# Optimization experiments

Measured on AMD Instinct MI355X. Metric: run time of the kernel, lower is better.

The kernel has to match this reference:

```python
import jax, jax.numpy as jnp
import numpy as np

# ---- fixed sizes ----
N_IN = 100_000          # total inner nodes
NODES_PER_INNER = 50    # nodes per inner graph
N_OUT = N_IN // NODES_PER_INNER          # 2000 outer nodes (= num inner graphs)
NODES_PER_OUTER = 125   # outer nodes per outer graph
B = N_OUT // NODES_PER_OUTER             # 16 graphs in the batch
DEG = 8
E_IN = N_IN * DEG        # 800_000 inner edges
E_OUT = N_OUT * DEG      # 16_000 outer edges
IN_FEATS = 64
OUT_FEATS = 64
H = 128                  # h_feats = [128]*6
NUM_CLASSES = 10


def _rand_edges(key, n_graphs, nodes_per_graph, edges_per_graph):
    """Random edges that stay inside each graph of a batched graph."""
    k1, k2 = jax.random.split(key)
    src_l = jax.random.randint(k1, (n_graphs, edges_per_graph), 0, nodes_per_graph)
    dst_l = jax.random.randint(k2, (n_graphs, edges_per_graph), 0, nodes_per_graph)
    off = (jnp.arange(n_graphs) * nodes_per_graph)[:, None]
    return ((src_l + off).reshape(-1).astype(jnp.int32),
            (dst_l + off).reshape(-1).astype(jnp.int32))


def setup_inputs() -> dict:
    key = jax.random.key(0)
    ks = jax.random.split(key, 24)
    inner_src, inner_dst = _rand_edges(ks[0], N_OUT, NODES_PER_INNER, E_IN // N_OUT)
    outer_src, outer_dst = _rand_edges(ks[1], B, NODES_PER_OUTER, E_OUT // B)

    def w(k, fan_in, fan_out):
        return jax.random.normal(k, (fan_in, fan_out), jnp.float32) * (1.0 / np.sqrt(fan_in))

    inp = {
        "in_layer_feat": jax.random.normal(ks[2], (N_IN, IN_FEATS), jnp.float32),
        "out_layer_feat": jax.random.normal(ks[3], (N_OUT, OUT_FEATS), jnp.float32),
        "inner_ew": jax.random.uniform(ks[4], (E_IN,), jnp.float32) + 0.5,
        "outer_ew": jax.random.uniform(ks[5], (E_OUT,), jnp.float32) + 0.5,
        "W1": w(ks[6], IN_FEATS, H),        "b1": jnp.zeros((H,), jnp.float32),
        "W2": w(ks[7], H, H),               "b2": jnp.zeros((H,), jnp.float32),
        "W3": w(ks[8], OUT_FEATS + H, H),   "b3": jnp.zeros((H,), jnp.float32),
        "W4": w(ks[9], H, H),               "b4": jnp.zeros((H,), jnp.float32),
        "W5": w(ks[10], H, H),              "b5": jnp.zeros((H,), jnp.float32),
        "W6": w(ks[11], H, H),              "b6": jnp.zeros((H,), jnp.float32),
        "Wc": w(ks[12], H, NUM_CLASSES),    "bc": jnp.zeros((NUM_CLASSES,), jnp.float32),
        "inner_src": inner_src, "inner_dst": inner_dst,
        "outer_src": outer_src, "outer_dst": outer_dst,
        "inner_node_graph": (jnp.arange(N_IN) // NODES_PER_INNER).astype(jnp.int32),
        "outer_node_graph": (jnp.arange(N_OUT) // NODES_PER_OUTER).astype(jnp.int32),
    }
    return inp


def graph_conv(src, dst, ew, x, W, b, n_nodes):
    """DGL GraphConv, norm='both', weighted aggregation, zero-in-degree allowed."""
    ones = jnp.ones(src.shape[0], x.dtype)
    deg_out = jnp.clip(jax.ops.segment_sum(ones, src, num_segments=n_nodes), 1.0)
    deg_in = jnp.clip(jax.ops.segment_sum(ones, dst, num_segments=n_nodes), 1.0)
    xs = x * jax.lax.rsqrt(deg_out)[:, None]                      # src normalization
    msg = xs[src] * ew[:, None]                                   # u_mul_e
    agg = jax.ops.segment_sum(msg, dst, num_segments=n_nodes)     # copy_e -> sum
    agg = agg * jax.lax.rsqrt(deg_in)[:, None]                    # dst normalization
    return agg @ W + b


def mean_nodes(h, node_graph, n_graphs, nodes_per_graph):
    return jax.ops.segment_sum(h, node_graph, num_segments=n_graphs) / nodes_per_graph


def reference(in_layer_feat, out_layer_feat, inner_ew, outer_ew,
              W1, b1, W2, b2, W3, b3, W4, b4, W5, b5, W6, b6, Wc, bc,
              inner_src, inner_dst, outer_src, outer_dst,
              inner_node_graph, outer_node_graph):
    # inner-graph message passing
    h = jax.nn.relu(graph_conv(inner_src, inner_dst, inner_ew, in_layer_feat, W1, b1, N_IN))
    h = jax.nn.relu(graph_conv(inner_src, inner_dst, inner_ew, h, W2, b2, N_IN))
    reduced = mean_nodes(h, inner_node_graph, N_OUT, float(NODES_PER_INNER))  # [N_OUT, H]
    merged = jnp.concatenate([out_layer_feat, reduced], axis=-1)              # [N_OUT, OUT_FEATS+H]
    # outer-graph message passing
    h = jax.nn.relu(graph_conv(outer_src, outer_dst, outer_ew, merged, W3, b3, N_OUT))
    h = jax.nn.relu(graph_conv(outer_src, outer_dst, outer_ew, h, W4, b4, N_OUT))
    h = jax.nn.relu(graph_conv(outer_src, outer_dst, outer_ew, h, W5, b5, N_OUT))
    h = jax.nn.relu(graph_conv(outer_src, outer_dst, outer_ew, h, W6, b6, N_OUT))
    hg = mean_nodes(h, outer_node_graph, B, float(NODES_PER_OUTER))           # [B, H]
    return hg @ Wc + bc                                                       # [B, NUM_CLASSES]
```

## Files before the change

kernel.cpp:

```cpp
#include <hip/hip_runtime.h>

#define NPI 50
#define EPI 400
#define NPO 125
#define EPO 1000
#define N_IN 100000
#define N_OUT 2000
#define NB 16
#define NC 10

typedef _Float16 half_t;
typedef _Float16 f16x8 __attribute__((ext_vector_type(8)));
typedef float f32x4 __attribute__((ext_vector_type(4)));

#define MFMA(a, b, c) __builtin_amdgcn_mfma_f32_16x16x32_f16(a, b, c, 0, 0, 0)

__device__ __forceinline__ f16x8 lds_ld8(const half_t* base, int row, int k, int strideB) {
    return *(const f16x8*)((const char*)base + row * strideB + ((k * 2) ^ ((row & 7) << 4)));
}
__device__ __forceinline__ void lds_st1(half_t* base, int row, int col, int strideB, float v) {
    *(half_t*)((char*)base + row * strideB + ((col * 2) ^ ((row & 7) << 4))) = (half_t)v;
}
__device__ __forceinline__ void lds_st1h(half_t* base, int row, int col, int strideB, half_t v) {
    *(half_t*)((char*)base + row * strideB + ((col * 2) ^ ((row & 7) << 4))) = v;
}
__device__ __forceinline__ f16x8 scr_ld8(const half_t* base, int row, int k) {
    return *(const f16x8*)((const char*)base + row * 64 + ((k * 2) ^ ((row & 3) << 4)));
}
__device__ __forceinline__ void scr_st1(half_t* base, int row, int col, float v) {
    *(half_t*)((char*)base + row * 64 + ((col * 2) ^ ((row & 3) << 4))) = (half_t)v;
}

__global__ __launch_bounds__(256) void k_pre(
    const float* __restrict__ W1, const float* __restrict__ W2,
    const float* __restrict__ W3, const float* __restrict__ W4,
    const float* __restrict__ W5, const float* __restrict__ W6,
    half_t* __restrict__ WT1, half_t* __restrict__ WT2,
    half_t* __restrict__ WT3, half_t* __restrict__ WT4,
    half_t* __restrict__ WT5, half_t* __restrict__ WT6,
    const float* __restrict__ ew, const int* __restrict__ esrc,
    const int* __restrict__ edst, half_t* __restrict__ Aout)
{
    __shared__ float Af[NPO * NPO];
    __shared__ int cO[NPO], cI[NPO];
    __shared__ float rso[NPO], rsi[NPO];
    const int t = threadIdx.x;

    if (blockIdx.x < 384) {
        int i = blockIdx.x * 256 + t;
        const float* src; half_t* dst; int K;
        if      (i < 8192)  { src = W1; dst = WT1; K = 64; }
        else if (i < 24576) { src = W2; dst = WT2; K = 128; i -= 8192; }
        else if (i < 49152) { src = W3; dst = WT3; K = 192; i -= 24576; }
        else if (i < 65536) { src = W4; dst = WT4; K = 128; i -= 49152; }
        else if (i < 81920) { src = W5; dst = WT5; K = 128; i -= 65536; }
        else                { src = W6; dst = WT6; K = 128; i -= 81920; }
        int c = i & 127, k = i >> 7;
        dst[c * K + k] = (half_t)src[k * 128 + c];
        return;
    }

    const int g = blockIdx.x - 384;
    const int nb = g * NPO, eb = g * EPO;
    for (int i = t; i < NPO * NPO; i += 256) Af[i] = 0.f;
    if (t < NPO) { cO[t] = 0; cI[t] = 0; }
    __syncthreads();
    for (int e = t; e < EPO; e += 256) {
        int s = esrc[eb + e] - nb, d = edst[eb + e] - nb;
        atomicAdd(&Af[d * NPO + s], ew[eb + e]);
        atomicAdd(&cO[s], 1); atomicAdd(&cI[d], 1);
    }
    __syncthreads();
    if (t < NPO) {
        rso[t] = rsqrtf((float)max(cO[t], 1));
        rsi[t] = rsqrtf((float)max(cI[t], 1));
    }
    __syncthreads();
    for (int i = t; i < 128 * 16; i += 256) {
        int d = i >> 4, s0 = (i & 15) * 8;
        f16x8 v;
        #pragma unroll
        for (int j = 0; j < 8; j++) {
            int s = s0 + j;
            float x = (d < NPO && s < NPO) ? Af[d * NPO + s] * rsi[d] * rso[s] : 0.f;
            v[j] = (half_t)x;
        }
        *(f16x8*)&Aout[(size_t)g * 16384 + d * 128 + s0] = v;
    }
}

__global__ __launch_bounds__(256, 5) void k_inner(
    const float* __restrict__ X, const float* __restrict__ outfeat,
    const float* __restrict__ ew, const int* __restrict__ esrc,
    const int* __restrict__ edst,
    const half_t* __restrict__ WT1, const float* __restrict__ b1,
    const half_t* __restrict__ WT2, const float* __restrict__ b2,
    half_t* __restrict__ merged)
{
    __shared__ alignas(16) char smem[21504];
    half_t* R2  = (half_t*)smem;
    float*  Af  = (float*)smem;
    half_t* scr = (half_t*)(smem + 16384);
    float*  pool= (float*)(smem + 20480);
    int*    cO  = (int*)(smem + 20992);
    int*    cI  = (int*)(smem + 21248);

    const int g = blockIdx.x, t = threadIdx.x;
    const int w = t >> 6, l = t & 63, lr = l & 15, lk = l >> 4;
    const int nb = g * NPI, eb = g * EPI;
    half_t* scrw = scr + w * 512;

    float ofv = (t < 64) ? outfeat[(size_t)g * 64 + t] : 0.f;
    int s0e, d0e; float w0e;
    { int e = eb + t; s0e = esrc[e] - nb; d0e = edst[e] - nb; w0e = ew[e]; }
    int s1e = 0, d1e = 0; float w1e = 0.f;
    const bool e1v = (t + 256 < EPI);
    if (e1v) { int e = eb + t + 256; s1e = esrc[e] - nb; d1e = edst[e] - nb; w1e = ew[e]; }
    const int srow = t >> 2, qc = t & 3;
    f16x8 xh0 = {}, xh1 = {};
    if (srow < NPI) {
        const float* xp = &X[(size_t)(nb + srow) * 64 + qc * 16];
        float4 a = *(const float4*)(xp + 0), b = *(const float4*)(xp + 4);
        float4 c = *(const float4*)(xp + 8), d = *(const float4*)(xp + 12);
        xh0[0]=(half_t)a.x; xh0[1]=(half_t)a.y; xh0[2]=(half_t)a.z; xh0[3]=(half_t)a.w;
        xh0[4]=(half_t)b.x; xh0[5]=(half_t)b.y; xh0[6]=(half_t)b.z; xh0[7]=(half_t)b.w;
        xh1[0]=(half_t)c.x; xh1[1]=(half_t)c.y; xh1[2]=(half_t)c.z; xh1[3]=(half_t)c.w;
        xh1[4]=(half_t)d.x; xh1[5]=(half_t)d.y; xh1[6]=(half_t)d.z; xh1[7]=(half_t)d.w;
    }

    if (t < 64) { cO[t] = 0; cI[t] = 0; }
    if (t >= 64 && t < 192) pool[t - 64] = 0.f;
    for (int i = t; i < 4096; i += 256) Af[i] = 0.f;
    __syncthreads();

    atomicAdd(&Af[d0e * 64 + (s0e ^ ((d0e & 7) << 2))], w0e);
    atomicAdd(&cO[s0e], 1); atomicAdd(&cI[d0e], 1);
    if (e1v) {
        atomicAdd(&Af[d1e * 64 + (s1e ^ ((d1e & 7) << 2))], w1e);
        atomicAdd(&cO[s1e], 1); atomicAdd(&cI[d1e], 1);
    }
    __syncthreads();

    f16x8 afr[2];
    {
        const int r = w * 16 + lr;
        const int sw = (r & 7) << 2;
        const float rsi_l = rsqrtf((float)max(cI[r], 1));
        #pragma unroll
        for (int ks = 0; ks < 2; ks++) {
            const int c0 = ks * 32 + lk * 8;
            f32x4 v0 = *(const f32x4*)&Af[r * 64 + (c0 ^ sw)];
            f32x4 v1 = *(const f32x4*)&Af[r * 64 + ((c0 + 4) ^ sw)];
            f16x8 fr;
            #pragma unroll
            for (int j = 0; j < 4; j++)
                fr[j] = (half_t)(v0[j] * rsi_l * rsqrtf((float)max(cO[c0 + j], 1)));
            #pragma unroll
            for (int j = 0; j < 4; j++)
                fr[4 + j] = (half_t)(v1[j] * rsi_l * rsqrtf((float)max(cO[c0 + 4 + j], 1)));
            afr[ks] = fr;
        }
    }
    __syncthreads();

    #pragma unroll
    for (int i = 0; i < 8; i++) lds_st1h(R2, qc * 16 + i, srow, 128, xh0[i]);
    #pragma unroll
    for (int i = 0; i < 8; i++) lds_st1h(R2, qc * 16 + 8 + i, srow, 128, xh1[i]);
    __syncthreads();

    f32x4 hacc[8] = {};
    #pragma unroll
    for (int kf = 0; kf < 2; kf++) {
        f16x8 wb[8];
        #pragma unroll
        for (int nt = 0; nt < 8; nt++)
            wb[nt] = *(const f16x8*)&WT1[(nt * 16 + lr) * 64 + kf * 32 + lk * 8];
        #pragma unroll
        for (int j = 0; j < 2; j++) {
            const int ft = kf * 2 + j;
            f32x4 tacc = {};
            #pragma unroll
            for (int ks = 0; ks < 2; ks++) {
                f16x8 b = lds_ld8(R2, ft * 16 + lr, ks * 32 + lk * 8, 128);
                tacc = MFMA(afr[ks], b, tacc);
            }
            #pragma unroll
            for (int q = 0; q < 4; q++) scr_st1(scrw, lk * 4 + q, j * 16 + lr, tacc[q]);
        }
        f16x8 a1 = scr_ld8(scrw, lr, lk * 8);
        #pragma unroll
        for (int nt = 0; nt < 8; nt++) hacc[nt] = MFMA(a1, wb[nt], hacc[nt]);
    }
    __syncthreads();
    #pragma unroll
    for (int nt = 0; nt < 8; nt++) {
        int c = nt * 16 + lr;
        float bb = b1[c];
        #pragma unroll
        for (int q = 0; q < 4; q++)
            lds_st1(R2, c, w * 16 + lk * 4 + q, 128, fmaxf(hacc[nt][q] + bb, 0.f));
    }
    __syncthreads();

    f32x4 h2[8] = {};
    #pragma unroll
    for (int kf = 0; kf < 4; kf++) {
        f16x8 wb[8];
        #pragma unroll
        for (int nt = 0; nt < 8; nt++)
            wb[nt] = *(const f16x8*)&WT2[(nt * 16 + lr) * 128 + kf * 32 + lk * 8];
        #pragma unroll
        for (int j = 0; j < 2; j++) {
            const int ft = kf * 2 + j;
            f32x4 tacc = {};
            #pragma unroll
            for (int ks = 0; ks < 2; ks++) {
                f16x8 b = lds_ld8(R2, ft * 16 + lr, ks * 32 + lk * 8, 128);
                tacc = MFMA(afr[ks], b, tacc);
            }
            #pragma unroll
            for (int q = 0; q < 4; q++) scr_st1(scrw, lk * 4 + q, j * 16 + lr, tacc[q]);
        }
        f16x8 a1 = scr_ld8(scrw, lr, lk * 8);
        #pragma unroll
        for (int nt = 0; nt < 8; nt++) h2[nt] = MFMA(a1, wb[nt], h2[nt]);
    }
    #pragma unroll
    for (int nt = 0; nt < 8; nt++) {
        int c = nt * 16 + lr;
        float bb = b2[c];
        float ps = 0.f;
        #pragma unroll
        for (int q = 0; q < 4; q++) {
            int m = w * 16 + lk * 4 + q;
            float v = fmaxf(h2[nt][q] + bb, 0.f);
            ps += (m < NPI) ? v : 0.f;
        }
        ps += __shfl_xor(ps, 16);
        ps += __shfl_xor(ps, 32);
        if (lk == 0) atomicAdd(&pool[c], ps);
    }
    __syncthreads();
    if (t < 64) merged[(size_t)g * 192 + t] = (half_t)ofv;
    else if (t < 192) merged[(size_t)g * 192 + t] = (half_t)(pool[t - 64] * (1.f / NPI));
}

template <int FIN, bool STAGE, bool LAST>
__device__ __forceinline__ void outer_layer(
    const f16x8* afr, const half_t* __restrict__ mg,
    const half_t* __restrict__ WT, const float* __restrict__ bias,
    half_t* bufP, half_t* bufQ, float* pool,
    int wr, int wc, int lr, int lk, int t)
{
    f32x4 hacc[4] = {};
    constexpr int NCH = FIN / 64;
    f16x8 hv[NCH];
    if constexpr (STAGE) {
        const int s = t >> 3, fo = (t & 7) * 8;
        #pragma unroll
        for (int ch = 0; ch < NCH; ch++) {
            f16x8 z = {};
            hv[ch] = (s < NPO) ? *(const f16x8*)&mg[(size_t)s * 192 + ch * 64 + fo] : z;
        }
    }
    #pragma unroll
    for (int ch = 0; ch < NCH; ch++) {
        f16x8 wtb[8];
        #pragma unroll
        for (int ks2 = 0; ks2 < 2; ks2++)
            #pragma unroll
            for (int nt = 0; nt < 4; nt++)
                wtb[ks2 * 4 + nt] = *(const f16x8*)&WT[
                    (size_t)(wc * 64 + nt * 16 + lr) * FIN + ch * 64 + ks2 * 32 + lk * 8];
        if constexpr (STAGE) {
            const int s = t >> 3, fo = (t & 7) * 8;
            #pragma unroll
            for (int j = 0; j < 8; j++) lds_st1h(bufP, fo + j, s, 256, hv[ch][j]);
            __syncthreads();
        }
        const int rb = STAGE ? 0 : ch * 64;
        f32x4 tacc[2] = {};
        #pragma unroll
        for (int ks = 0; ks < 4; ks++) {
            #pragma unroll
            for (int nt = 0; nt < 2; nt++) {
                f16x8 b = lds_ld8(bufP, rb + wc * 32 + nt * 16 + lr, ks * 32 + lk * 8, 256);
                tacc[nt] = MFMA(afr[ks], b, tacc[nt]);
            }
        }
        #pragma unroll
        for (int nt = 0; nt < 2; nt++)
            #pragma unroll
            for (int q = 0; q < 4; q++)
                lds_st1(bufQ, wr * 16 + lk * 4 + q, wc * 32 + nt * 16 + lr, 128,
                        tacc[nt][q]);
        __syncthreads();
        #pragma unroll
        for (int ks2 = 0; ks2 < 2; ks2++) {
            f16x8 a1 = lds_ld8(bufQ, wr * 16 + lr, ks2 * 32 + lk * 8, 128);
            #pragma unroll
            for (int nt = 0; nt < 4; nt++)
                hacc[nt] = MFMA(a1, wtb[ks2 * 4 + nt], hacc[nt]);
        }
        __syncthreads();
    }
    if constexpr (!LAST) {
        #pragma unroll
        for (int nt = 0; nt < 4; nt++) {
            int c = wc * 64 + nt * 16 + lr;
            float bb = bias[c];
            #pragma unroll
            for (int q = 0; q < 4; q++)
                lds_st1(bufP, c, wr * 16 + lk * 4 + q, 256, fmaxf(hacc[nt][q] + bb, 0.f));
        }
        __syncthreads();
    } else {
        #pragma unroll
        for (int nt = 0; nt < 4; nt++) {
            int c = wc * 64 + nt * 16 + lr;
            float bb = bias[c];
            float ps = 0.f;
            #pragma unroll
            for (int q = 0; q < 4; q++) {
                int d = wr * 16 + lk * 4 + q;
                float v = fmaxf(hacc[nt][q] + bb, 0.f);
                ps += (d < NPO) ? v : 0.f;
            }
            ps += __shfl_xor(ps, 16);
            ps += __shfl_xor(ps, 32);
            if (lk == 0) atomicAdd(&pool[c], ps);
        }
        __syncthreads();
    }
}

__global__ __launch_bounds__(1024) void k_outer(
    const half_t* __restrict__ Aout, const half_t* __restrict__ merged,
    const half_t* __restrict__ WT3, const float* __restrict__ b3,
    const half_t* __restrict__ WT4, const float* __restrict__ b4,
    const half_t* __restrict__ WT5, const float* __restrict__ b5,
    const half_t* __restrict__ WT6, const float* __restrict__ b6,
    const float* __restrict__ Wc, const float* __restrict__ bc,
    float* __restrict__ out)
{
    __shared__ alignas(16) char smem[49704];
    half_t* bufP = (half_t*)smem;
    half_t* bufQ = (half_t*)(smem + 32768);
    float*  pool = (float*)(smem + 49152);
    float*  cls  = (float*)(smem + 49664);

    const int g = blockIdx.x, t = threadIdx.x;
    const int w = t >> 6, l = t & 63, lr = l & 15, lk = l >> 4;
    const int wr = w & 7, wc = w >> 3;
    const half_t* mg = merged + (size_t)g * NPO * 192;

    f16x8 afr[4];
    #pragma unroll
    for (int ks = 0; ks < 4; ks++)
        afr[ks] = *(const f16x8*)&Aout[(size_t)g * 16384
                                       + (wr * 16 + lr) * 128 + ks * 32 + lk * 8];
    if (t < 128) pool[t] = 0.f;
    if (t >= 128 && t < 128 + NC) cls[t - 128] = 0.f;
    __syncthreads();

    outer_layer<192, true,  false>(afr, mg, WT3, b3, bufP, bufQ, pool, wr, wc, lr, lk, t);
    outer_layer<128, false, false>(afr, nullptr, WT4, b4, bufP, bufQ, pool, wr, wc, lr, lk, t);
    outer_layer<128, false, false>(afr, nullptr, WT5, b5, bufP, bufQ, pool, wr, wc, lr, lk, t);
    outer_layer<128, false, true >(afr, nullptr, WT6, b6, bufP, bufQ, pool, wr, wc, lr, lk, t);

    if (t < 128) {
        float val = pool[t] * (1.f / NPO);
        float p[NC];
        #pragma unroll
        for (int c = 0; c < NC; c++) p[c] = val * Wc[t * NC + c];
        #pragma unroll
        for (int off = 32; off >= 1; off >>= 1)
            #pragma unroll
            for (int c = 0; c < NC; c++) p[c] += __shfl_xor(p[c], off);
        if ((t & 63) == 0)
            #pragma unroll
            for (int c = 0; c < NC; c++) atomicAdd(&cls[c], p[c]);
    }
    __syncthreads();
    if (t < NC) out[g * NC + t] = cls[t] + bc[t];
}

extern "C" void kernel_launch(void* const* d_in, const int* in_sizes, int n_in,
                              void* d_out, int out_size, void* d_ws, size_t ws_size,
                              hipStream_t stream)
{
    const float* X       = (const float*)d_in[0];
    const float* outfeat = (const float*)d_in[1];
    const float* iew     = (const float*)d_in[2];
    const float* oew     = (const float*)d_in[3];
    const float* W1 = (const float*)d_in[4];  const float* b1 = (const float*)d_in[5];
    const float* W2 = (const float*)d_in[6];  const float* b2 = (const float*)d_in[7];
    const float* W3 = (const float*)d_in[8];  const float* b3 = (const float*)d_in[9];
    const float* W4 = (const float*)d_in[10]; const float* b4 = (const float*)d_in[11];
    const float* W5 = (const float*)d_in[12]; const float* b5 = (const float*)d_in[13];
    const float* W6 = (const float*)d_in[14]; const float* b6 = (const float*)d_in[15];
    const float* Wc = (const float*)d_in[16]; const float* bc = (const float*)d_in[17];
    const int* isrc = (const int*)d_in[18];   const int* idst = (const int*)d_in[19];
    const int* osrc = (const int*)d_in[20];   const int* odst = (const int*)d_in[21];

    char* base = (char*)d_ws;
    half_t* WT1 = (half_t*)(base + 0);
    half_t* WT2 = (half_t*)(base + 16384);
    half_t* WT3 = (half_t*)(base + 49152);
    half_t* WT4 = (half_t*)(base + 98304);
    half_t* WT5 = (half_t*)(base + 131072);
    half_t* WT6 = (half_t*)(base + 163840);
    half_t* AoutG  = (half_t*)(base + 196608);
    half_t* merged = (half_t*)(base + 720896);

    k_pre<<<400, 256, 0, stream>>>(W1, W2, W3, W4, W5, W6,
                                   WT1, WT2, WT3, WT4, WT5, WT6,
                                   oew, osrc, odst, AoutG);
    k_inner<<<N_OUT, 256, 0, stream>>>(X, outfeat, iew, isrc, idst,
                                       WT1, b1, WT2, b2, merged);
    k_outer<<<NB, 1024, 0, stream>>>(AoutG, merged, WT3, b3, WT4, b4,
                                     WT5, b5, WT6, b6, Wc, bc, (float*)d_out);
}
```

Baseline: 122.3 us.

## Assign one inner graph per wavefront and drop block-level barriers

The inner-graph kernel now processes each inner graph with a single 64-lane wavefront, packing two graphs per 128-thread block, instead of a 256-thread block per graph. Each wave owns private LDS regions, so all __syncthreads and the pooled LDS atomics go away, and the mean pooling is done in registers with shuffles. Each wave loops over four 16-row tiles and keeps the adjacency fragments for all tiles in registers, with output-degree normalisation factors precomputed. This removes cross-wave barrier stalls, but it raises register pressure and LDS per block, lowers the number of waves per graph, and leans on wave-lockstep execution for LDS ordering.

```diff
diff --git a/kernel.cpp b/kernel.cpp
--- a/kernel.cpp
+++ b/kernel.cpp
@@ -89,7 +89,7 @@
     }
 }
 
-__global__ __launch_bounds__(256, 5) void k_inner(
+__global__ __launch_bounds__(128, 2) void k_inner(
     const float* __restrict__ X, const float* __restrict__ outfeat,
     const float* __restrict__ ew, const int* __restrict__ esrc,
     const int* __restrict__ edst,
@@ -97,53 +97,55 @@
     const half_t* __restrict__ WT2, const float* __restrict__ b2,
     half_t* __restrict__ merged)
 {
-    __shared__ alignas(16) char smem[21504];
-    half_t* R2  = (half_t*)smem;
-    float*  Af  = (float*)smem;
-    half_t* scr = (half_t*)(smem + 16384);
-    float*  pool= (float*)(smem + 20480);
-    int*    cO  = (int*)(smem + 20992);
-    int*    cI  = (int*)(smem + 21248);
-
-    const int g = blockIdx.x, t = threadIdx.x;
-    const int w = t >> 6, l = t & 63, lr = l & 15, lk = l >> 4;
+    __shared__ alignas(16) char smem[52224];
+    const int t = threadIdx.x, w = t >> 6, l = t & 63;
+    const int lr = l & 15, lk = l >> 4;
+    const int g = blockIdx.x * 2 + w;
+    char* R = smem + w * 26112;
+    float*  Af   = (float*)R;
+    half_t* h1T  = (half_t*)R;
+    half_t* XT   = (half_t*)(R + 16384);
+    half_t* scrw = (half_t*)(R + 24576);
+    int*    cO   = (int*)(R + 25600);
+    int*    cI   = (int*)(R + 25856);
     const int nb = g * NPI, eb = g * EPI;
-    half_t* scrw = scr + w * 512;
-
-    float ofv = (t < 64) ? outfeat[(size_t)g * 64 + t] : 0.f;
-    int s0e, d0e; float w0e;
-    { int e = eb + t; s0e = esrc[e] - nb; d0e = edst[e] - nb; w0e = ew[e]; }
-    int s1e = 0, d1e = 0; float w1e = 0.f;
-    const bool e1v = (t + 256 < EPI);
-    if (e1v) { int e = eb + t + 256; s1e = esrc[e] - nb; d1e = edst[e] - nb; w1e = ew[e]; }
-    const int srow = t >> 2, qc = t & 3;
-    f16x8 xh0 = {}, xh1 = {};
-    if (srow < NPI) {
-        const float* xp = &X[(size_t)(nb + srow) * 64 + qc * 16];
-        float4 a = *(const float4*)(xp + 0), b = *(const float4*)(xp + 4);
-        float4 c = *(const float4*)(xp + 8), d = *(const float4*)(xp + 12);
-        xh0[0]=(half_t)a.x; xh0[1]=(half_t)a.y; xh0[2]=(half_t)a.z; xh0[3]=(half_t)a.w;
-        xh0[4]=(half_t)b.x; xh0[5]=(half_t)b.y; xh0[6]=(half_t)b.z; xh0[7]=(half_t)b.w;
-        xh1[0]=(half_t)c.x; xh1[1]=(half_t)c.y; xh1[2]=(half_t)c.z; xh1[3]=(half_t)c.w;
-        xh1[4]=(half_t)d.x; xh1[5]=(half_t)d.y; xh1[6]=(half_t)d.z; xh1[7]=(half_t)d.w;
-    }
-
-    if (t < 64) { cO[t] = 0; cI[t] = 0; }
-    if (t >= 64 && t < 192) pool[t - 64] = 0.f;
-    for (int i = t; i < 4096; i += 256) Af[i] = 0.f;
-    __syncthreads();
-
-    atomicAdd(&Af[d0e * 64 + (s0e ^ ((d0e & 7) << 2))], w0e);
-    atomicAdd(&cO[s0e], 1); atomicAdd(&cI[d0e], 1);
-    if (e1v) {
-        atomicAdd(&Af[d1e * 64 + (s1e ^ ((d1e & 7) << 2))], w1e);
-        atomicAdd(&cO[s1e], 1); atomicAdd(&cI[d1e], 1);
-    }
-    __syncthreads();
-
-    f16x8 afr[2];
-    {
-        const int r = w * 16 + lr;
+
+    float ofv = outfeat[(size_t)g * 64 + l];
+    int se[7], de[7]; float wgt[7];
+    #pragma unroll
+    for (int i = 0; i < 7; i++) {
+        int e = l + i * 64;
+        if (e < EPI) {
+            se[i] = esrc[eb + e] - nb; de[i] = edst[eb + e] - nb; wgt[i] = ew[eb + e];
+        } else { se[i] = 0; de[i] = 0; wgt[i] = 0.f; }
+    }
+    float bb1[8], bb2[8];
+    #pragma unroll
+    for (int nt = 0; nt < 8; nt++) { bb1[nt] = b1[nt * 16 + lr]; bb2[nt] = b2[nt * 16 + lr]; }
+
+    cO[l] = 0; cI[l] = 0;
+    #pragma unroll
+    for (int i = 0; i < 16; i++)
+        *(f32x4*)&Af[(i * 64 + l) * 4] = (f32x4){0.f, 0.f, 0.f, 0.f};
+    #pragma unroll
+    for (int i = 0; i < 7; i++) {
+        if (l + i * 64 < EPI) {
+            atomicAdd(&Af[de[i] * 64 + (se[i] ^ ((de[i] & 7) << 2))], wgt[i]);
+            atomicAdd(&cO[se[i]], 1); atomicAdd(&cI[de[i]], 1);
+        }
+    }
+
+    float rso8[2][8];
+    #pragma unroll
+    for (int ks = 0; ks < 2; ks++)
+        #pragma unroll
+        for (int j = 0; j < 8; j++)
+            rso8[ks][j] = rsqrtf((float)max(cO[ks * 32 + lk * 8 + j], 1));
+
+    f16x8 afr[4][2];
+    #pragma unroll
+    for (int st = 0; st < 4; st++) {
+        const int r = st * 16 + lr;
         const int sw = (r & 7) << 2;
         const float rsi_l = rsqrtf((float)max(cI[r], 1));
         #pragma unroll
@@ -153,97 +155,109 @@
             f32x4 v1 = *(const f32x4*)&Af[r * 64 + ((c0 + 4) ^ sw)];
             f16x8 fr;
             #pragma unroll
-            for (int j = 0; j < 4; j++)
-                fr[j] = (half_t)(v0[j] * rsi_l * rsqrtf((float)max(cO[c0 + j], 1)));
-            #pragma unroll
-            for (int j = 0; j < 4; j++)
-                fr[4 + j] = (half_t)(v1[j] * rsi_l * rsqrtf((float)max(cO[c0 + 4 + j], 1)));
-            afr[ks] = fr;
-        }
-    }
-    __syncthreads();
-
-    #pragma unroll
-    for (int i = 0; i < 8; i++) lds_st1h(R2, qc * 16 + i, srow, 128, xh0[i]);
-    #pragma unroll
-    for (int i = 0; i < 8; i++) lds_st1h(R2, qc * 16 + 8 + i, srow, 128, xh1[i]);
-    __syncthreads();
-
-    f32x4 hacc[8] = {};
-    #pragma unroll
-    for (int kf = 0; kf < 2; kf++) {
-        f16x8 wb[8];
+            for (int j = 0; j < 4; j++) fr[j] = (half_t)(v0[j] * rsi_l * rso8[ks][j]);
+            #pragma unroll
+            for (int j = 0; j < 4; j++) fr[4 + j] = (half_t)(v1[j] * rsi_l * rso8[ks][4 + j]);
+            afr[st][ks] = fr;
+        }
+    }
+
+    #pragma unroll
+    for (int i = 0; i < 8; i++)
+        *(f32x4*)((char*)XT + (i * 64 + l) * 16) = (f32x4){0.f, 0.f, 0.f, 0.f};
+    for (int i = l; i < NPI * 16; i += 64) {
+        int row = i >> 4, c4 = (i & 15) * 4;
+        float4 xv = *(const float4*)&X[(size_t)(nb + row) * 64 + c4];
+        lds_st1h(XT, c4 + 0, row, 128, (half_t)xv.x);
+        lds_st1h(XT, c4 + 1, row, 128, (half_t)xv.y);
+        lds_st1h(XT, c4 + 2, row, 128, (half_t)xv.z);
+        lds_st1h(XT, c4 + 3, row, 128, (half_t)xv.w);
+    }
+
+    #pragma unroll
+    for (int st = 0; st < 4; st++) {
+        f32x4 hacc[8] = {};
+        #pragma unroll
+        for (int kf = 0; kf < 2; kf++) {
+            f16x8 wb[8];
+            #pragma unroll
+            for (int nt = 0; nt < 8; nt++)
+                wb[nt] = *(const f16x8*)&WT1[(nt * 16 + lr) * 64 + kf * 32 + lk * 8];
+            #pragma unroll
+            for (int j = 0; j < 2; j++) {
+                const int ft = kf * 2 + j;
+                f32x4 tacc = {};
+                #pragma unroll
+                for (int ks = 0; ks < 2; ks++) {
+                    f16x8 b = lds_ld8(XT, ft * 16 + lr, ks * 32 + lk * 8, 128);
+                    tacc = MFMA(afr[st][ks], b, tacc);
+                }
+                #pragma unroll
+                for (int q = 0; q < 4; q++) scr_st1(scrw, lk * 4 + q, j * 16 + lr, tacc[q]);
+            }
+            f16x8 a1 = scr_ld8(scrw, lr, lk * 8);
+            #pragma unroll
+            for (int nt = 0; nt < 8; nt++) hacc[nt] = MFMA(a1, wb[nt], hacc[nt]);
+        }
+        #pragma unroll
+        for (int nt = 0; nt < 8; nt++) {
+            int c = nt * 16 + lr;
+            #pragma unroll
+            for (int q = 0; q < 4; q++)
+                lds_st1(h1T, c, st * 16 + lk * 4 + q, 128,
+                        fmaxf(hacc[nt][q] + bb1[nt], 0.f));
+        }
+    }
+
+    float psum[8];
+    #pragma unroll
+    for (int nt = 0; nt < 8; nt++) psum[nt] = 0.f;
+    #pragma unroll
+    for (int st = 0; st < 4; st++) {
+        f32x4 h2acc[8] = {};
+        #pragma unroll
+        for (int kf = 0; kf < 4; kf++) {
+            f16x8 wb[8];
+            #pragma unroll
+            for (int nt = 0; nt < 8; nt++)
+                wb[nt] = *(const f16x8*)&WT2[(nt * 16 + lr) * 128 + kf * 32 + lk * 8];
+            #pragma unroll
+            for (int j = 0; j < 2; j++) {
+                const int ft = kf * 2 + j;
+                f32x4 tacc = {};
+                #pragma unroll
+                for (int ks = 0; ks < 2; ks++) {
+                    f16x8 b = lds_ld8(h1T, ft * 16 + lr, ks * 32 + lk * 8, 128);
+                    tacc = MFMA(afr[st][ks], b, tacc);
+                }
+                #pragma unroll
+                for (int q = 0; q < 4; q++) scr_st1(scrw, lk * 4 + q, j * 16 + lr, tacc[q]);
+            }
+            f16x8 a1 = scr_ld8(scrw, lr, lk * 8);
+            #pragma unroll
+            for (int nt = 0; nt < 8; nt++) h2acc[nt] = MFMA(a1, wb[nt], h2acc[nt]);
+        }
+        #pragma unroll
+        for (int nt = 0; nt < 8; nt++) {
+            #pragma unroll
+            for (int q = 0; q < 4; q++) {
+                int r = st * 16 + lk * 4 + q;
+                float v = fmaxf(h2acc[nt][q] + bb2[nt], 0.f);
+                psum[nt] += (r < NPI) ? v : 0.f;
+            }
+        }
+    }
+    #pragma unroll
+    for (int nt = 0; nt < 8; nt++) {
+        psum[nt] += __shfl_xor(psum[nt], 16);
+        psum[nt] += __shfl_xor(psum[nt], 32);
+    }
+    merged[(size_t)g * 192 + l] = (half_t)ofv;
+    if (l < 16) {
         #pragma unroll
         for (int nt = 0; nt < 8; nt++)
-            wb[nt] = *(const f16x8*)&WT1[(nt * 16 + lr) * 64 + kf * 32 + lk * 8];
-        #pragma unroll
-        for (int j = 0; j < 2; j++) {
-            const int ft = kf * 2 + j;
-            f32x4 tacc = {};
-            #pragma unroll
-            for (int ks = 0; ks < 2; ks++) {
-                f16x8 b = lds_ld8(R2, ft * 16 + lr, ks * 32 + lk * 8, 128);
-                tacc = MFMA(afr[ks], b, tacc);
-            }
-            #pragma unroll
-            for (int q = 0; q < 4; q++) scr_st1(scrw, lk * 4 + q, j * 16 + lr, tacc[q]);
-        }
-        f16x8 a1 = scr_ld8(scrw, lr, lk * 8);
-        #pragma unroll
-        for (int nt = 0; nt < 8; nt++) hacc[nt] = MFMA(a1, wb[nt], hacc[nt]);
-    }
-    __syncthreads();
-    #pragma unroll
-    for (int nt = 0; nt < 8; nt++) {
-        int c = nt * 16 + lr;
-        float bb = b1[c];
-        #pragma unroll
-        for (int q = 0; q < 4; q++)
-            lds_st1(R2, c, w * 16 + lk * 4 + q, 128, fmaxf(hacc[nt][q] + bb, 0.f));
-    }
-    __syncthreads();
-
-    f32x4 h2[8] = {};
-    #pragma unroll
-    for (int kf = 0; kf < 4; kf++) {
-        f16x8 wb[8];
-        #pragma unroll
-        for (int nt = 0; nt < 8; nt++)
-            wb[nt] = *(const f16x8*)&WT2[(nt * 16 + lr) * 128 + kf * 32 + lk * 8];
-        #pragma unroll
-        for (int j = 0; j < 2; j++) {
-            const int ft = kf * 2 + j;
-            f32x4 tacc = {};
-            #pragma unroll
-            for (int ks = 0; ks < 2; ks++) {
-                f16x8 b = lds_ld8(R2, ft * 16 + lr, ks * 32 + lk * 8, 128);
-                tacc = MFMA(afr[ks], b, tacc);
-            }
-            #pragma unroll
-            for (int q = 0; q < 4; q++) scr_st1(scrw, lk * 4 + q, j * 16 + lr, tacc[q]);
-        }
-        f16x8 a1 = scr_ld8(scrw, lr, lk * 8);
-        #pragma unroll
-        for (int nt = 0; nt < 8; nt++) h2[nt] = MFMA(a1, wb[nt], h2[nt]);
-    }
-    #pragma unroll
-    for (int nt = 0; nt < 8; nt++) {
-        int c = nt * 16 + lr;
-        float bb = b2[c];
-        float ps = 0.f;
-        #pragma unroll
-        for (int q = 0; q < 4; q++) {
-            int m = w * 16 + lk * 4 + q;
-            float v = fmaxf(h2[nt][q] + bb, 0.f);
-            ps += (m < NPI) ? v : 0.f;
-        }
-        ps += __shfl_xor(ps, 16);
-        ps += __shfl_xor(ps, 32);
-        if (lk == 0) atomicAdd(&pool[c], ps);
-    }
-    __syncthreads();
-    if (t < 64) merged[(size_t)g * 192 + t] = (half_t)ofv;
-    else if (t < 192) merged[(size_t)g * 192 + t] = (half_t)(pool[t - 64] * (1.f / NPI));
+            merged[(size_t)g * 192 + 64 + nt * 16 + l] = (half_t)(psum[nt] * (1.f / NPI));
+    }
 }
 
 template <int FIN, bool STAGE, bool LAST>
@@ -417,8 +431,8 @@
     k_pre<<<400, 256, 0, stream>>>(W1, W2, W3, W4, W5, W6,
                                    WT1, WT2, WT3, WT4, WT5, WT6,
                                    oew, osrc, odst, AoutG);
-    k_inner<<<N_OUT, 256, 0, stream>>>(X, outfeat, iew, isrc, idst,
-                                       WT1, b1, WT2, b2, merged);
+    k_inner<<<N_OUT / 2, 128, 0, stream>>>(X, outfeat, iew, isrc, idst,
+                                           WT1, b1, WT2, b2, merged);
     k_outer<<<NB, 1024, 0, stream>>>(AoutG, merged, WT3, b3, WT4, b4,
                                      WT5, b5, WT6, b6, Wc, bc, (float*)d_out);
 }
```

Result: no change. 120.6 us (-1.3%).
